# Optimization experiments

Measured on AMD Instinct MI355X. Metric: run time of the kernel, lower is better.

Reference implementation:

```python
import jax, jax.numpy as jnp
import numpy as np


def setup_inputs() -> dict:
    key = jax.random.key(0)
    ks = jax.random.split(key, 6)
    T, B, I, H = 256, 64, 1024, 1024
    x = jax.random.normal(ks[0], (T, B, I), dtype=jnp.float32)
    h0 = jax.random.normal(ks[1], (B, H), dtype=jnp.float32)
    c0 = jax.random.normal(ks[2], (B, H), dtype=jnp.float32)
    # LSTMCell params: _W [I+H, 4H] (xavier-like scale), _b zeros
    W = jax.random.normal(ks[3], (I + H, 4 * H), dtype=jnp.float32) * (2.0 / (I + H + 4 * H)) ** 0.5
    b = jnp.zeros((4 * H,), dtype=jnp.float32)
    L = jax.random.randint(ks[4], (B,), 0, T, dtype=jnp.int64 if jax.config.jax_enable_x64 else jnp.int32)
    return {"x": x, "h0": h0, "c0": c0, "W": W, "b": b, "L": L}


def reference(x, h0, c0, W, b, L):
    # RNN(cell_type='lstm', num_layers=1, batch_first=False) forward.
    # x: [T, B, I]; h0, c0: [B, H]; W: [I+H, 4H]; b: [4H]; L: [B] lengths.
    T = x.shape[0]
    H = h0.shape[-1]

    def step(carry, inp):
        h_, c_ = carry
        xt, t = inp  # xt: [B, I]
        cand = jnp.concatenate([xt, h_], axis=-1) @ W + b  # [B, 4H]
        i, f, o, g = jnp.split(cand, 4, axis=-1)
        c_new = jax.nn.sigmoid(i) * jnp.tanh(g) + jax.nn.sigmoid(f) * c_
        h_new = jax.nn.sigmoid(o) * jnp.tanh(c_new)
        mask = (t < L)[:, None]  # [B, 1]; freeze state past sequence end
        h = jnp.where(mask, h_new, h_)
        c = jnp.where(mask, c_new, c_)
        return (h, c), h

    (_, _), out = jax.lax.scan(step, (h0, c0), (x, jnp.arange(T)))
    return out  # [T, B, H]
```

## Files before the change

### kernel.cpp

```cpp
#include <hip/hip_runtime.h>
#include <stdint.h>

typedef unsigned short u16;
typedef unsigned int u32;
typedef unsigned long long u64;
typedef __attribute__((ext_vector_type(8))) short bf16x8;
typedef __attribute__((ext_vector_type(4))) float f32x4;
typedef __attribute__((ext_vector_type(4))) u16 u16x4;

#define T_STEPS 256
#define BATCH 64
#define IDIM 1024
#define HDIM 1024
#define NBLK 256
#define NJ 4
#define KPAD 2056
#define THREADS 512
#define FLAG_LINE_U32 16
#define GO_U32 (NBLK * FLAG_LINE_U32)
#define X_OFF 262144
#define H_OFF (X_OFF + T_STEPS * BATCH * IDIM * 2)
#define LDS_BYTES 83712

static __device__ __forceinline__ u16 f2bf(float f) {
  u32 u = __builtin_bit_cast(u32, f);
  u += 0x7FFFu + ((u >> 16) & 1u);
  return (u16)(u >> 16);
}
static __device__ __forceinline__ float sigf(float x) {
  return __builtin_amdgcn_rcpf(1.f + __expf(-x));
}
static __device__ __forceinline__ float tanhf_(float x) {
  float ax = __builtin_fabsf(x);
  float e = __expf(-2.f * ax);
  float t = 1.f - 2.f * e * __builtin_amdgcn_rcpf(1.f + e);
  return __builtin_copysignf(t, x);
}

static __device__ __forceinline__ void gwait(u32* flags, u32* go, u32 e,
                                             int bid, int tid, int lane) {
  if (bid == 0) {
    if ((tid >> 6) == 7) {
      const u32* p0 = &flags[lane * FLAG_LINE_U32];
      const u32* p1 = &flags[(lane + 64) * FLAG_LINE_U32];
      const u32* p2 = &flags[(lane + 128) * FLAG_LINE_U32];
      const u32* p3 = &flags[(lane + 192) * FLAG_LINE_U32];
      while (true) {
        u32 a = __hip_atomic_load(p0, __ATOMIC_RELAXED, __HIP_MEMORY_SCOPE_AGENT);
        u32 b = __hip_atomic_load(p1, __ATOMIC_RELAXED, __HIP_MEMORY_SCOPE_AGENT);
        u32 c = __hip_atomic_load(p2, __ATOMIC_RELAXED, __HIP_MEMORY_SCOPE_AGENT);
        u32 d = __hip_atomic_load(p3, __ATOMIC_RELAXED, __HIP_MEMORY_SCOPE_AGENT);
        int mine = (a >= e) && (b >= e) && (c >= e) && (d >= e);
        if (__all(mine)) break;
        __builtin_amdgcn_s_sleep(1);
      }
      if (lane < 8)
        __hip_atomic_store(&go[lane * FLAG_LINE_U32], e, __ATOMIC_RELAXED,
                           __HIP_MEMORY_SCOPE_AGENT);
    }
  } else {
    if (tid == 448) {
      while (__hip_atomic_load(&go[(bid & 7) * FLAG_LINE_U32], __ATOMIC_RELAXED,
                               __HIP_MEMORY_SCOPE_AGENT) < e)
        __builtin_amdgcn_s_sleep(2);
    }
  }
  if (tid == 448)
    __builtin_amdgcn_fence(__ATOMIC_ACQUIRE, "agent");
  __syncthreads();
}

static __device__ __forceinline__ void gbar_heavy(u32* flags, u32* go, int bid,
                                                  int tid) {
  __syncthreads();
  if (tid == 0) {
    __threadfence();
    __hip_atomic_store(&flags[bid * FLAG_LINE_U32], 1u, __ATOMIC_RELAXED,
                       __HIP_MEMORY_SCOPE_AGENT);
  }
  if (bid == 0) {
    if (tid < NBLK) {
      while (__hip_atomic_load(&flags[tid * FLAG_LINE_U32], __ATOMIC_RELAXED,
                               __HIP_MEMORY_SCOPE_AGENT) < 1u)
        __builtin_amdgcn_s_sleep(1);
    }
    __syncthreads();
    if (tid < 8)
      __hip_atomic_store(&go[tid * FLAG_LINE_U32], 1u, __ATOMIC_RELAXED,
                         __HIP_MEMORY_SCOPE_AGENT);
  } else {
    if (tid == 0) {
      while (__hip_atomic_load(&go[(bid & 7) * FLAG_LINE_U32], __ATOMIC_RELAXED,
                               __HIP_MEMORY_SCOPE_AGENT) < 1u)
        __builtin_amdgcn_s_sleep(2);
    }
  }
  if (tid == 0) __threadfence();
  __syncthreads();
}

__global__ __launch_bounds__(THREADS, 2)
void lstm_persistent(const float* __restrict__ x, const float* __restrict__ h0,
                     const float* __restrict__ c0, const float* __restrict__ W,
                     const float* __restrict__ bias, const int* __restrict__ L,
                     float* __restrict__ out, u16* __restrict__ xbf,
                     u16* __restrict__ hbuf, u32* __restrict__ flags) {
  extern __shared__ char smem[];
  u16* Wlds = (u16*)smem;
  float* cand = (float*)(smem + 65792);
  u16* hstage = (u16*)(smem + 83200);

  u32* go = flags + GO_U32;

  const int bid = blockIdx.x;
  const int tid = threadIdx.x;
  const int wave = tid >> 6;
  const int lane = tid & 63;
  const int q = lane >> 4;
  const int ln = lane & 15;
  const int mh = wave & 1;
  const int kh = wave >> 1;

  {
    const int gtid = bid * THREADS + tid;
    const f32x4* xv = (const f32x4*)x;
    u16x4* ov = (u16x4*)xbf;
#pragma unroll
    for (int it = 0; it < 32; ++it) {
      int i = gtid + it * (NBLK * THREADS);
      f32x4 v = xv[i];
      u16x4 o;
      o[0] = f2bf(v[0]); o[1] = f2bf(v[1]); o[2] = f2bf(v[2]); o[3] = f2bf(v[3]);
      ov[i] = o;
    }
    if (gtid < BATCH * HDIM) hbuf[BATCH * HDIM + gtid] = f2bf(h0[gtid]);
  }

  {
    const int g = tid & 3;
    const int kq2 = tid >> 2;
    const f32x4* Wv = (const f32x4*)W;
#pragma unroll 4
    for (int i = 0; i < 16; ++i) {
      int k = kq2 + 128 * i;
      f32x4 w4 = Wv[(size_t)k * 1024 + g * 256 + bid];
#pragma unroll
      for (int jj = 0; jj < 4; ++jj)
        Wlds[(g * 4 + jj) * KPAD + k] = f2bf(w4[jj]);
    }
  }

  float c_reg = 0.f, h_reg = 0.f, b_i = 0.f, b_f = 0.f, b_o = 0.f, b_g = 0.f;
  int Lb = 0, pb = 0, pj = 0;
  if (tid < 256) {
    pb = tid >> 2;
    pj = tid & 3;
    int gj = bid * NJ + pj;
    Lb = L[pb];
    c_reg = c0[pb * HDIM + gj];
    h_reg = h0[pb * HDIM + gj];
    b_i = bias[0 * HDIM + gj];
    b_f = bias[1 * HDIM + gj];
    b_o = bias[2 * HDIM + gj];
    b_g = bias[3 * HDIM + gj];
  }

  gbar_heavy(flags, go, bid, tid);

  const int arow = 32 * mh + ln;
  const bool fromx = (kh < 2);
  const int kbase = (kh & 1) * 512;
  const u16* wp = &Wlds[ln * KPAD + kh * 512 + q * 8];

  for (int t = 0; t < T_STEPS; ++t) {
    f32x4 acc0 = {0.f, 0.f, 0.f, 0.f};
    f32x4 acc1 = {0.f, 0.f, 0.f, 0.f};
    if (fromx) {
      const u16* pa0 =
          xbf + (size_t)t * (BATCH * IDIM) + arow * 1024 + kbase + q * 8;
      const u16* pa1 = pa0 + 16 * 1024;
#pragma unroll
      for (int ks = 0; ks < 16; ++ks) {
        bf16x8 a0 = *(const bf16x8*)(pa0 + ks * 32);
        bf16x8 a1 = *(const bf16x8*)(pa1 + ks * 32);
        bf16x8 bw = *(const bf16x8*)(wp + ks * 32);
        acc0 = __builtin_amdgcn_mfma_f32_16x16x32_bf16(a0, bw, acc0, 0, 0, 0);
        acc1 = __builtin_amdgcn_mfma_f32_16x16x32_bf16(a1, bw, acc1, 0, 0, 0);
      }
    }
    asm volatile("" ::"v"(acc0), "v"(acc1));
    __builtin_amdgcn_sched_barrier(0);

    if (t > 0) gwait(flags, go, (u32)(t + 1), bid, tid, lane);

    if (!fromx) {
      const u16* pa0 = hbuf + ((t + 1) & 1) * (BATCH * HDIM) + arow * 1024 +
                       kbase + q * 8;
      const u16* pa1 = pa0 + 16 * 1024;
#pragma unroll
      for (int ks = 0; ks < 16; ++ks) {
        bf16x8 a0 = *(const bf16x8*)(pa0 + ks * 32);
        bf16x8 a1 = *(const bf16x8*)(pa1 + ks * 32);
        bf16x8 bw = *(const bf16x8*)(wp + ks * 32);
        acc0 = __builtin_amdgcn_mfma_f32_16x16x32_bf16(a0, bw, acc0, 0, 0, 0);
        acc1 = __builtin_amdgcn_mfma_f32_16x16x32_bf16(a1, bw, acc1, 0, 0, 0);
      }
    }
    {
      float* c0p = &cand[(kh * 64 + 32 * mh + q * 4) * 17 + ln];
      float* c1p = c0p + 16 * 17;
#pragma unroll
      for (int r = 0; r < 4; ++r) {
        c0p[r * 17] = acc0[r];
        c1p[r * 17] = acc1[r];
      }
    }
    __syncthreads();
    if (tid < 256) {
      float vi = b_i, vf = b_f, vo = b_o, vg = b_g;
#pragma unroll
      for (int p = 0; p < 4; ++p) {
        const float* cp = &cand[(p * 64 + pb) * 17];
        vi += cp[pj];
        vf += cp[4 + pj];
        vo += cp[8 + pj];
        vg += cp[12 + pj];
      }
      float ig = sigf(vi), fg = sigf(vf), og = sigf(vo), gg = tanhf_(vg);
      float cn = ig * gg + fg * c_reg;
      float hn = og * tanhf_(cn);
      if (t < Lb) { c_reg = cn; h_reg = hn; }
      hstage[tid] = f2bf(h_reg);
    }
    __syncthreads();
    if (t < T_STEPS - 1) {
      if (tid < 64) {
        u64 v = ((const u64*)hstage)[tid];
        u64* dst =
            (u64*)(hbuf + (t & 1) * (BATCH * HDIM) + tid * HDIM + bid * NJ);
        __hip_atomic_store(dst, v, __ATOMIC_RELAXED, __HIP_MEMORY_SCOPE_AGENT);
      }
      __syncthreads();
      if (tid == 0)
        __hip_atomic_store(&flags[bid * FLAG_LINE_U32], (u32)(t + 2),
                           __ATOMIC_RELAXED, __HIP_MEMORY_SCOPE_AGENT);
    }
    if (tid < 256)
      __hip_atomic_store(&out[((size_t)t * BATCH + pb) * HDIM + bid * NJ + pj],
                         h_reg, __ATOMIC_RELAXED, __HIP_MEMORY_SCOPE_AGENT);
  }
}

extern "C" void kernel_launch(void* const* d_in, const int* in_sizes, int n_in,
                              void* d_out, int out_size, void* d_ws, size_t ws_size,
                              hipStream_t stream) {
  (void)in_sizes; (void)n_in; (void)out_size; (void)ws_size;
  const float* x = (const float*)d_in[0];
  const float* h0 = (const float*)d_in[1];
  const float* c0 = (const float*)d_in[2];
  const float* W = (const float*)d_in[3];
  const float* bias = (const float*)d_in[4];
  const int* L = (const int*)d_in[5];
  float* out = (float*)d_out;

  char* ws = (char*)d_ws;
  u32* flags = (u32*)ws;
  u16* xbf = (u16*)(ws + X_OFF);
  u16* hbuf = (u16*)(ws + H_OFF);

  hipFuncSetAttribute(reinterpret_cast<const void*>(lstm_persistent),
                      hipFuncAttributeMaxDynamicSharedMemorySize, 160 * 1024);
  hipMemsetAsync(ws, 0, 32768, stream);
  hipLaunchKernelGGL(lstm_persistent, dim3(NBLK), dim3(THREADS), LDS_BYTES,
                     stream, x, h0, c0, W, bias, L, out, xbf, hbuf, flags);
}
```

Baseline: 2.612 ms.

## Replace centralized grid barrier with per-wave fine-grained flag polling on producer blocks

Drops the block-0 aggregator barrier. Each wave that consumes h now polls only the 128 producer-block flags covering its K slice, in groups of 32, and starts the MFMAs for a group as soon as that group is ready. The h reads become relaxed atomic loads so they bypass stale cache, the output store moves earlier, and a __syncthreads before the flag publish is replaced by a waitcnt. This aims to cut barrier latency and overlap waiting with compute. The trade-offs are heavier flag polling traffic and a possible ordering risk, because the flag store by tid 0 is no longer fenced against stores from other threads.

```diff
diff --git a/kernel.cpp b/kernel.cpp
--- a/kernel.cpp
+++ b/kernel.cpp
@@ -7,6 +7,7 @@
 typedef __attribute__((ext_vector_type(8))) short bf16x8;
 typedef __attribute__((ext_vector_type(4))) float f32x4;
 typedef __attribute__((ext_vector_type(4))) u16 u16x4;
+typedef __attribute__((ext_vector_type(2))) u64 u64x2;
 
 #define T_STEPS 256
 #define BATCH 64
@@ -37,39 +38,6 @@
   return __builtin_copysignf(t, x);
 }
 
-static __device__ __forceinline__ void gwait(u32* flags, u32* go, u32 e,
-                                             int bid, int tid, int lane) {
-  if (bid == 0) {
-    if ((tid >> 6) == 7) {
-      const u32* p0 = &flags[lane * FLAG_LINE_U32];
-      const u32* p1 = &flags[(lane + 64) * FLAG_LINE_U32];
-      const u32* p2 = &flags[(lane + 128) * FLAG_LINE_U32];
-      const u32* p3 = &flags[(lane + 192) * FLAG_LINE_U32];
-      while (true) {
-        u32 a = __hip_atomic_load(p0, __ATOMIC_RELAXED, __HIP_MEMORY_SCOPE_AGENT);
-        u32 b = __hip_atomic_load(p1, __ATOMIC_RELAXED, __HIP_MEMORY_SCOPE_AGENT);
-        u32 c = __hip_atomic_load(p2, __ATOMIC_RELAXED, __HIP_MEMORY_SCOPE_AGENT);
-        u32 d = __hip_atomic_load(p3, __ATOMIC_RELAXED, __HIP_MEMORY_SCOPE_AGENT);
-        int mine = (a >= e) && (b >= e) && (c >= e) && (d >= e);
-        if (__all(mine)) break;
-        __builtin_amdgcn_s_sleep(1);
-      }
-      if (lane < 8)
-        __hip_atomic_store(&go[lane * FLAG_LINE_U32], e, __ATOMIC_RELAXED,
-                           __HIP_MEMORY_SCOPE_AGENT);
-    }
-  } else {
-    if (tid == 448) {
-      while (__hip_atomic_load(&go[(bid & 7) * FLAG_LINE_U32], __ATOMIC_RELAXED,
-                               __HIP_MEMORY_SCOPE_AGENT) < e)
-        __builtin_amdgcn_s_sleep(2);
-    }
-  }
-  if (tid == 448)
-    __builtin_amdgcn_fence(__ATOMIC_ACQUIRE, "agent");
-  __syncthreads();
-}
-
 static __device__ __forceinline__ void gbar_heavy(u32* flags, u32* go, int bid,
                                                   int tid) {
   __syncthreads();
@@ -170,6 +138,7 @@
   const int arow = 32 * mh + ln;
   const bool fromx = (kh < 2);
   const int kbase = (kh & 1) * 512;
+  const int pbase = kbase >> 2;
   const u16* wp = &Wlds[ln * KPAD + kh * 512 + q * 8];
 
   for (int t = 0; t < T_STEPS; ++t) {
@@ -187,23 +156,45 @@
         acc0 = __builtin_amdgcn_mfma_f32_16x16x32_bf16(a0, bw, acc0, 0, 0, 0);
         acc1 = __builtin_amdgcn_mfma_f32_16x16x32_bf16(a1, bw, acc1, 0, 0, 0);
       }
-    }
-    asm volatile("" ::"v"(acc0), "v"(acc1));
-    __builtin_amdgcn_sched_barrier(0);
-
-    if (t > 0) gwait(flags, go, (u32)(t + 1), bid, tid, lane);
-
-    if (!fromx) {
+    } else {
+      const u32 e = (u32)(t + 1);
       const u16* pa0 = hbuf + ((t + 1) & 1) * (BATCH * HDIM) + arow * 1024 +
                        kbase + q * 8;
       const u16* pa1 = pa0 + 16 * 1024;
-#pragma unroll
-      for (int ks = 0; ks < 16; ++ks) {
-        bf16x8 a0 = *(const bf16x8*)(pa0 + ks * 32);
-        bf16x8 a1 = *(const bf16x8*)(pa1 + ks * 32);
-        bf16x8 bw = *(const bf16x8*)(wp + ks * 32);
-        acc0 = __builtin_amdgcn_mfma_f32_16x16x32_bf16(a0, bw, acc0, 0, 0, 0);
-        acc1 = __builtin_amdgcn_mfma_f32_16x16x32_bf16(a1, bw, acc1, 0, 0, 0);
+      u32 fv = __hip_atomic_load(
+          &flags[(pbase + (lane & 31)) * FLAG_LINE_U32], __ATOMIC_RELAXED,
+          __HIP_MEMORY_SCOPE_AGENT);
+#pragma unroll
+      for (int g = 0; g < 4; ++g) {
+        while (!__all(fv >= e)) {
+          __builtin_amdgcn_s_sleep(1);
+          fv = __hip_atomic_load(
+              &flags[(pbase + g * 32 + (lane & 31)) * FLAG_LINE_U32],
+              __ATOMIC_RELAXED, __HIP_MEMORY_SCOPE_AGENT);
+        }
+        u32 fnext = e;
+        if (g < 3)
+          fnext = __hip_atomic_load(
+              &flags[(pbase + (g + 1) * 32 + (lane & 31)) * FLAG_LINE_U32],
+              __ATOMIC_RELAXED, __HIP_MEMORY_SCOPE_AGENT);
+#pragma unroll
+        for (int ks = g * 4; ks < g * 4 + 4; ++ks) {
+          u64x2 r0, r1;
+          r0[0] = __hip_atomic_load((const u64*)(pa0 + ks * 32),
+                                    __ATOMIC_RELAXED, __HIP_MEMORY_SCOPE_AGENT);
+          r0[1] = __hip_atomic_load((const u64*)(pa0 + ks * 32 + 4),
+                                    __ATOMIC_RELAXED, __HIP_MEMORY_SCOPE_AGENT);
+          r1[0] = __hip_atomic_load((const u64*)(pa1 + ks * 32),
+                                    __ATOMIC_RELAXED, __HIP_MEMORY_SCOPE_AGENT);
+          r1[1] = __hip_atomic_load((const u64*)(pa1 + ks * 32 + 4),
+                                    __ATOMIC_RELAXED, __HIP_MEMORY_SCOPE_AGENT);
+          bf16x8 a0 = __builtin_bit_cast(bf16x8, r0);
+          bf16x8 a1 = __builtin_bit_cast(bf16x8, r1);
+          bf16x8 bw = *(const bf16x8*)(wp + ks * 32);
+          acc0 = __builtin_amdgcn_mfma_f32_16x16x32_bf16(a0, bw, acc0, 0, 0, 0);
+          acc1 = __builtin_amdgcn_mfma_f32_16x16x32_bf16(a1, bw, acc1, 0, 0, 0);
+        }
+        fv = fnext;
       }
     }
     {
@@ -230,6 +221,8 @@
       float cn = ig * gg + fg * c_reg;
       float hn = og * tanhf_(cn);
       if (t < Lb) { c_reg = cn; h_reg = hn; }
+      __hip_atomic_store(&out[((size_t)t * BATCH + pb) * HDIM + bid * NJ + pj],
+                         h_reg, __ATOMIC_RELAXED, __HIP_MEMORY_SCOPE_AGENT);
       hstage[tid] = f2bf(h_reg);
     }
     __syncthreads();
@@ -239,15 +232,12 @@
         u64* dst =
             (u64*)(hbuf + (t & 1) * (BATCH * HDIM) + tid * HDIM + bid * NJ);
         __hip_atomic_store(dst, v, __ATOMIC_RELAXED, __HIP_MEMORY_SCOPE_AGENT);
-      }
-      __syncthreads();
+        asm volatile("s_waitcnt vmcnt(0)" ::: "memory");
+      }
       if (tid == 0)
         __hip_atomic_store(&flags[bid * FLAG_LINE_U32], (u32)(t + 2),
                            __ATOMIC_RELAXED, __HIP_MEMORY_SCOPE_AGENT);
     }
-    if (tid < 256)
-      __hip_atomic_store(&out[((size_t)t * BATCH + pb) * HDIM + bid * NJ + pj],
-                         h_reg, __ATOMIC_RELAXED, __HIP_MEMORY_SCOPE_AGENT);
   }
 }
 
```

Result: slower. 3.443 ms (+31.8%).

## Split LSTM step work by batch rows across waves, drop LDS reduction

Applied to the files above, without the earlier changes.

Blocks shrink from 512 to 256 threads. Each of the four waves now owns 16 batch rows and runs the full K range over both x and h, instead of waves splitting K and combining partials through an LDS candidate buffer. The gate values are exchanged with lane shuffles, and each wave applies the LSTM update in registers and writes its own packed h slice, which removes two __syncthreads and the LDS round trip from every timestep. In exchange, each wave issues twice as many MFMAs serially after the global wait, so the h-dependent critical path per step is longer.

```diff
diff --git a/kernel.cpp b/kernel.cpp
--- a/kernel.cpp
+++ b/kernel.cpp
@@ -15,12 +15,12 @@
 #define NBLK 256
 #define NJ 4
 #define KPAD 2056
-#define THREADS 512
+#define THREADS 256
 #define FLAG_LINE_U32 16
 #define GO_U32 (NBLK * FLAG_LINE_U32)
 #define X_OFF 262144
 #define H_OFF (X_OFF + T_STEPS * BATCH * IDIM * 2)
-#define LDS_BYTES 83712
+#define LDS_BYTES 65792
 
 static __device__ __forceinline__ u16 f2bf(float f) {
   u32 u = __builtin_bit_cast(u32, f);
@@ -40,7 +40,7 @@
 static __device__ __forceinline__ void gwait(u32* flags, u32* go, u32 e,
                                              int bid, int tid, int lane) {
   if (bid == 0) {
-    if ((tid >> 6) == 7) {
+    if ((tid >> 6) == 3) {
       const u32* p0 = &flags[lane * FLAG_LINE_U32];
       const u32* p1 = &flags[(lane + 64) * FLAG_LINE_U32];
       const u32* p2 = &flags[(lane + 128) * FLAG_LINE_U32];
@@ -59,13 +59,13 @@
                            __HIP_MEMORY_SCOPE_AGENT);
     }
   } else {
-    if (tid == 448) {
+    if (tid == 192) {
       while (__hip_atomic_load(&go[(bid & 7) * FLAG_LINE_U32], __ATOMIC_RELAXED,
                                __HIP_MEMORY_SCOPE_AGENT) < e)
         __builtin_amdgcn_s_sleep(2);
     }
   }
-  if (tid == 448)
+  if (tid == 192)
     __builtin_amdgcn_fence(__ATOMIC_ACQUIRE, "agent");
   __syncthreads();
 }
@@ -99,7 +99,7 @@
   __syncthreads();
 }
 
-__global__ __launch_bounds__(THREADS, 2)
+__global__ __launch_bounds__(THREADS, 1)
 void lstm_persistent(const float* __restrict__ x, const float* __restrict__ h0,
                      const float* __restrict__ c0, const float* __restrict__ W,
                      const float* __restrict__ bias, const int* __restrict__ L,
@@ -107,26 +107,22 @@
                      u16* __restrict__ hbuf, u32* __restrict__ flags) {
   extern __shared__ char smem[];
   u16* Wlds = (u16*)smem;
-  float* cand = (float*)(smem + 65792);
-  u16* hstage = (u16*)(smem + 83200);
 
   u32* go = flags + GO_U32;
 
   const int bid = blockIdx.x;
   const int tid = threadIdx.x;
-  const int wave = tid >> 6;
+  const int m = tid >> 6;
   const int lane = tid & 63;
   const int q = lane >> 4;
   const int ln = lane & 15;
-  const int mh = wave & 1;
-  const int kh = wave >> 1;
 
   {
     const int gtid = bid * THREADS + tid;
     const f32x4* xv = (const f32x4*)x;
     u16x4* ov = (u16x4*)xbf;
 #pragma unroll
-    for (int it = 0; it < 32; ++it) {
+    for (int it = 0; it < 64; ++it) {
       int i = gtid + it * (NBLK * THREADS);
       f32x4 v = xv[i];
       u16x4 o;
@@ -141,8 +137,8 @@
     const int kq2 = tid >> 2;
     const f32x4* Wv = (const f32x4*)W;
 #pragma unroll 4
-    for (int i = 0; i < 16; ++i) {
-      int k = kq2 + 128 * i;
+    for (int i = 0; i < 32; ++i) {
+      int k = kq2 + 64 * i;
       f32x4 w4 = Wv[(size_t)k * 1024 + g * 256 + bid];
 #pragma unroll
       for (int jj = 0; jj < 4; ++jj)
@@ -150,42 +146,45 @@
     }
   }
 
-  float c_reg = 0.f, h_reg = 0.f, b_i = 0.f, b_f = 0.f, b_o = 0.f, b_g = 0.f;
-  int Lb = 0, pb = 0, pj = 0;
-  if (tid < 256) {
-    pb = tid >> 2;
-    pj = tid & 3;
-    int gj = bid * NJ + pj;
-    Lb = L[pb];
-    c_reg = c0[pb * HDIM + gj];
-    h_reg = h0[pb * HDIM + gj];
+  const bool act = (ln < 4);
+  float c_reg[4], h_reg[4];
+  int Lb[4];
+  float b_i = 0.f, b_f = 0.f, b_o = 0.f, b_g = 0.f;
+#pragma unroll
+  for (int r = 0; r < 4; ++r) { c_reg[r] = 0.f; h_reg[r] = 0.f; Lb[r] = 0; }
+  if (act) {
+    const int gj = bid * NJ + ln;
     b_i = bias[0 * HDIM + gj];
     b_f = bias[1 * HDIM + gj];
     b_o = bias[2 * HDIM + gj];
     b_g = bias[3 * HDIM + gj];
+#pragma unroll
+    for (int r = 0; r < 4; ++r) {
+      const int b = 16 * m + 4 * q + r;
+      Lb[r] = L[b];
+      c_reg[r] = c0[b * HDIM + gj];
+      h_reg[r] = h0[b * HDIM + gj];
+    }
   }
 
   gbar_heavy(flags, go, bid, tid);
 
-  const int arow = 32 * mh + ln;
-  const bool fromx = (kh < 2);
-  const int kbase = (kh & 1) * 512;
-  const u16* wp = &Wlds[ln * KPAD + kh * 512 + q * 8];
+  const u16* wp = &Wlds[ln * KPAD + q * 8];
 
   for (int t = 0; t < T_STEPS; ++t) {
     f32x4 acc0 = {0.f, 0.f, 0.f, 0.f};
     f32x4 acc1 = {0.f, 0.f, 0.f, 0.f};
-    if (fromx) {
-      const u16* pa0 =
-          xbf + (size_t)t * (BATCH * IDIM) + arow * 1024 + kbase + q * 8;
-      const u16* pa1 = pa0 + 16 * 1024;
-#pragma unroll
-      for (int ks = 0; ks < 16; ++ks) {
-        bf16x8 a0 = *(const bf16x8*)(pa0 + ks * 32);
-        bf16x8 a1 = *(const bf16x8*)(pa1 + ks * 32);
+    {
+      const u16* pax =
+          xbf + (size_t)t * (BATCH * IDIM) + (16 * m + ln) * 1024 + q * 8;
+#pragma unroll
+      for (int ks = 0; ks < 32; ++ks) {
+        bf16x8 a = *(const bf16x8*)(pax + ks * 32);
         bf16x8 bw = *(const bf16x8*)(wp + ks * 32);
-        acc0 = __builtin_amdgcn_mfma_f32_16x16x32_bf16(a0, bw, acc0, 0, 0, 0);
-        acc1 = __builtin_amdgcn_mfma_f32_16x16x32_bf16(a1, bw, acc1, 0, 0, 0);
+        if (ks & 1)
+          acc1 = __builtin_amdgcn_mfma_f32_16x16x32_bf16(a, bw, acc1, 0, 0, 0);
+        else
+          acc0 = __builtin_amdgcn_mfma_f32_16x16x32_bf16(a, bw, acc0, 0, 0, 0);
       }
     }
     asm volatile("" ::"v"(acc0), "v"(acc1));
@@ -193,61 +192,67 @@
 
     if (t > 0) gwait(flags, go, (u32)(t + 1), bid, tid, lane);
 
-    if (!fromx) {
-      const u16* pa0 = hbuf + ((t + 1) & 1) * (BATCH * HDIM) + arow * 1024 +
-                       kbase + q * 8;
-      const u16* pa1 = pa0 + 16 * 1024;
-#pragma unroll
-      for (int ks = 0; ks < 16; ++ks) {
-        bf16x8 a0 = *(const bf16x8*)(pa0 + ks * 32);
-        bf16x8 a1 = *(const bf16x8*)(pa1 + ks * 32);
-        bf16x8 bw = *(const bf16x8*)(wp + ks * 32);
-        acc0 = __builtin_amdgcn_mfma_f32_16x16x32_bf16(a0, bw, acc0, 0, 0, 0);
-        acc1 = __builtin_amdgcn_mfma_f32_16x16x32_bf16(a1, bw, acc1, 0, 0, 0);
-      }
-    }
     {
-      float* c0p = &cand[(kh * 64 + 32 * mh + q * 4) * 17 + ln];
-      float* c1p = c0p + 16 * 17;
+      const u16* pah = hbuf + ((t + 1) & 1) * (BATCH * HDIM) +
+                       (16 * m + ln) * 1024 + q * 8;
+      const u16* wph = wp + 1024;
+#pragma unroll
+      for (int ks = 0; ks < 32; ++ks) {
+        bf16x8 a = *(const bf16x8*)(pah + ks * 32);
+        bf16x8 bw = *(const bf16x8*)(wph + ks * 32);
+        if (ks & 1)
+          acc1 = __builtin_amdgcn_mfma_f32_16x16x32_bf16(a, bw, acc1, 0, 0, 0);
+        else
+          acc0 = __builtin_amdgcn_mfma_f32_16x16x32_bf16(a, bw, acc0, 0, 0, 0);
+      }
+    }
+    f32x4 s = acc0 + acc1;
+    float sf[4], so[4], sg[4];
+#pragma unroll
+    for (int r = 0; r < 4; ++r) {
+      sf[r] = __shfl_xor(s[r], 4);
+      so[r] = __shfl_xor(s[r], 8);
+      sg[r] = __shfl_xor(s[r], 12);
+    }
+    if (act) {
 #pragma unroll
       for (int r = 0; r < 4; ++r) {
-        c0p[r * 17] = acc0[r];
-        c1p[r * 17] = acc1[r];
-      }
-    }
-    __syncthreads();
-    if (tid < 256) {
-      float vi = b_i, vf = b_f, vo = b_o, vg = b_g;
-#pragma unroll
-      for (int p = 0; p < 4; ++p) {
-        const float* cp = &cand[(p * 64 + pb) * 17];
-        vi += cp[pj];
-        vf += cp[4 + pj];
-        vo += cp[8 + pj];
-        vg += cp[12 + pj];
-      }
-      float ig = sigf(vi), fg = sigf(vf), og = sigf(vo), gg = tanhf_(vg);
-      float cn = ig * gg + fg * c_reg;
-      float hn = og * tanhf_(cn);
-      if (t < Lb) { c_reg = cn; h_reg = hn; }
-      hstage[tid] = f2bf(h_reg);
-    }
-    __syncthreads();
+        float vi = s[r] + b_i, vf = sf[r] + b_f, vo = so[r] + b_o,
+              vg = sg[r] + b_g;
+        float ig = sigf(vi), fg = sigf(vf), og = sigf(vo), gg = tanhf_(vg);
+        float cn = ig * gg + fg * c_reg[r];
+        float hn = og * tanhf_(cn);
+        if (t < Lb[r]) { c_reg[r] = cn; h_reg[r] = hn; }
+      }
+    }
     if (t < T_STEPS - 1) {
-      if (tid < 64) {
-        u64 v = ((const u64*)hstage)[tid];
-        u64* dst =
-            (u64*)(hbuf + (t & 1) * (BATCH * HDIM) + tid * HDIM + bid * NJ);
-        __hip_atomic_store(dst, v, __ATOMIC_RELAXED, __HIP_MEMORY_SCOPE_AGENT);
+      u32 v[4];
+#pragma unroll
+      for (int r = 0; r < 4; ++r) v[r] = (u32)f2bf(h_reg[r]);
+#pragma unroll
+      for (int r = 0; r < 4; ++r) {
+        u32 a32 = v[r] | (((u32)__shfl_xor((int)v[r], 1)) << 16);
+        u32 b32 = (u32)__shfl_xor((int)a32, 2);
+        if (ln == 0) {
+          u64 w = (u64)a32 | ((u64)b32 << 32);
+          u64* dst = (u64*)(hbuf + (t & 1) * (BATCH * HDIM) +
+                            (16 * m + 4 * q + r) * HDIM + bid * NJ);
+          __hip_atomic_store(dst, w, __ATOMIC_RELAXED,
+                             __HIP_MEMORY_SCOPE_AGENT);
+        }
       }
       __syncthreads();
       if (tid == 0)
         __hip_atomic_store(&flags[bid * FLAG_LINE_U32], (u32)(t + 2),
                            __ATOMIC_RELAXED, __HIP_MEMORY_SCOPE_AGENT);
     }
-    if (tid < 256)
-      __hip_atomic_store(&out[((size_t)t * BATCH + pb) * HDIM + bid * NJ + pj],
-                         h_reg, __ATOMIC_RELAXED, __HIP_MEMORY_SCOPE_AGENT);
+    if (act) {
+#pragma unroll
+      for (int r = 0; r < 4; ++r)
+        __hip_atomic_store(
+            &out[((size_t)t * BATCH + 16 * m + 4 * q + r) * HDIM + bid * NJ + ln],
+            h_reg[r], __ATOMIC_RELAXED, __HIP_MEMORY_SCOPE_AGENT);
+    }
   }
 }
 
```

After: 2.903 ms. +11.1%, slower.

## Split K across all waves for both x and h, block-contiguous h layout

Applied to the files above, without the earlier changes.

Each wave now covers a quarter of both the x and the h reduction, instead of half the waves doing x only and half doing h only. The serial post-barrier h-dependent work per wave is halved, which shortens the critical path of each recurrent step. The h buffer is stored in a [j/4][batch][4] layout so every block writes one contiguous 512-byte chunk. Readers now gather 8-byte pieces with strided loads. The cand reduction indexing is adjusted to match the new wave-to-K mapping.

```diff
diff --git a/kernel.cpp b/kernel.cpp
--- a/kernel.cpp
+++ b/kernel.cpp
@@ -7,6 +7,7 @@
 typedef __attribute__((ext_vector_type(8))) short bf16x8;
 typedef __attribute__((ext_vector_type(4))) float f32x4;
 typedef __attribute__((ext_vector_type(4))) u16 u16x4;
+typedef __attribute__((ext_vector_type(2))) u64 u64x2;
 
 #define T_STEPS 256
 #define BATCH 64
@@ -119,7 +120,8 @@
   const int q = lane >> 4;
   const int ln = lane & 15;
   const int mh = wave & 1;
-  const int kh = wave >> 1;
+  const int kq = wave >> 1;
+  const int arow = 32 * mh + ln;
 
   {
     const int gtid = bid * THREADS + tid;
@@ -133,7 +135,10 @@
       o[0] = f2bf(v[0]); o[1] = f2bf(v[1]); o[2] = f2bf(v[2]); o[3] = f2bf(v[3]);
       ov[i] = o;
     }
-    if (gtid < BATCH * HDIM) hbuf[BATCH * HDIM + gtid] = f2bf(h0[gtid]);
+    if (gtid < BATCH * HDIM) {
+      int b = gtid >> 10, j = gtid & 1023;
+      hbuf[BATCH * HDIM + (j >> 2) * 256 + b * 4 + (j & 3)] = f2bf(h0[gtid]);
+    }
   }
 
   {
@@ -167,23 +172,21 @@
 
   gbar_heavy(flags, go, bid, tid);
 
-  const int arow = 32 * mh + ln;
-  const bool fromx = (kh < 2);
-  const int kbase = (kh & 1) * 512;
-  const u16* wp = &Wlds[ln * KPAD + kh * 512 + q * 8];
+  const u16* wpx = &Wlds[ln * KPAD + kq * 256 + q * 8];
+  const u16* wph = &Wlds[ln * KPAD + 1024 + kq * 256 + q * 8];
 
   for (int t = 0; t < T_STEPS; ++t) {
     f32x4 acc0 = {0.f, 0.f, 0.f, 0.f};
     f32x4 acc1 = {0.f, 0.f, 0.f, 0.f};
-    if (fromx) {
+    {
       const u16* pa0 =
-          xbf + (size_t)t * (BATCH * IDIM) + arow * 1024 + kbase + q * 8;
+          xbf + (size_t)t * (BATCH * IDIM) + arow * 1024 + kq * 256 + q * 8;
       const u16* pa1 = pa0 + 16 * 1024;
 #pragma unroll
-      for (int ks = 0; ks < 16; ++ks) {
+      for (int ks = 0; ks < 8; ++ks) {
         bf16x8 a0 = *(const bf16x8*)(pa0 + ks * 32);
         bf16x8 a1 = *(const bf16x8*)(pa1 + ks * 32);
-        bf16x8 bw = *(const bf16x8*)(wp + ks * 32);
+        bf16x8 bw = *(const bf16x8*)(wpx + ks * 32);
         acc0 = __builtin_amdgcn_mfma_f32_16x16x32_bf16(a0, bw, acc0, 0, 0, 0);
         acc1 = __builtin_amdgcn_mfma_f32_16x16x32_bf16(a1, bw, acc1, 0, 0, 0);
       }
@@ -193,21 +196,26 @@
 
     if (t > 0) gwait(flags, go, (u32)(t + 1), bid, tid, lane);
 
-    if (!fromx) {
-      const u16* pa0 = hbuf + ((t + 1) & 1) * (BATCH * HDIM) + arow * 1024 +
-                       kbase + q * 8;
-      const u16* pa1 = pa0 + 16 * 1024;
-#pragma unroll
-      for (int ks = 0; ks < 16; ++ks) {
-        bf16x8 a0 = *(const bf16x8*)(pa0 + ks * 32);
-        bf16x8 a1 = *(const bf16x8*)(pa1 + ks * 32);
-        bf16x8 bw = *(const bf16x8*)(wp + ks * 32);
+    {
+      const u16* hb = hbuf + ((t + 1) & 1) * (BATCH * HDIM) + kq * (256 * 64) +
+                      q * (2 * 256);
+#pragma unroll
+      for (int ks = 0; ks < 8; ++ks) {
+        const u16* c0p_ = hb + ks * (8 * 256);
+        u64x2 r0, r1;
+        r0[0] = *(const u64*)(c0p_ + arow * 4);
+        r0[1] = *(const u64*)(c0p_ + 256 + arow * 4);
+        r1[0] = *(const u64*)(c0p_ + (arow + 16) * 4);
+        r1[1] = *(const u64*)(c0p_ + 256 + (arow + 16) * 4);
+        bf16x8 a0 = __builtin_bit_cast(bf16x8, r0);
+        bf16x8 a1 = __builtin_bit_cast(bf16x8, r1);
+        bf16x8 bw = *(const bf16x8*)(wph + ks * 32);
         acc0 = __builtin_amdgcn_mfma_f32_16x16x32_bf16(a0, bw, acc0, 0, 0, 0);
         acc1 = __builtin_amdgcn_mfma_f32_16x16x32_bf16(a1, bw, acc1, 0, 0, 0);
       }
     }
     {
-      float* c0p = &cand[(kh * 64 + 32 * mh + q * 4) * 17 + ln];
+      float* c0p = &cand[(wave * 32 + q * 4) * 17 + ln];
       float* c1p = c0p + 16 * 17;
 #pragma unroll
       for (int r = 0; r < 4; ++r) {
@@ -217,10 +225,11 @@
     }
     __syncthreads();
     if (tid < 256) {
+      const int mhp = pb >> 5, lr = pb & 31;
       float vi = b_i, vf = b_f, vo = b_o, vg = b_g;
 #pragma unroll
       for (int p = 0; p < 4; ++p) {
-        const float* cp = &cand[(p * 64 + pb) * 17];
+        const float* cp = &cand[((p * 2 + mhp) * 32 + lr) * 17];
         vi += cp[pj];
         vf += cp[4 + pj];
         vo += cp[8 + pj];
@@ -237,7 +246,7 @@
       if (tid < 64) {
         u64 v = ((const u64*)hstage)[tid];
         u64* dst =
-            (u64*)(hbuf + (t & 1) * (BATCH * HDIM) + tid * HDIM + bid * NJ);
+            (u64*)(hbuf + (t & 1) * (BATCH * HDIM) + bid * 256 + tid * 4);
         __hip_atomic_store(dst, v, __ATOMIC_RELAXED, __HIP_MEMORY_SCOPE_AGENT);
       }
       __syncthreads();
```

New measurement: 2.478 ms. -5.1%, faster.
